# Kernel optimization log

Hardware: AMD Instinct MI355X
Metric: run time of the kernel (lower is better)

The kernel has to match this reference:

```python
import jax, jax.numpy as jnp
import numpy as np

N = 4096      # batch of RNA sequences
SEQ = 41      # hardcoded sequence length in the torch code
VEC = 15      # vector_length
T = 8         # target_length
EMB = 32      # embedding_dim of RNASequenceFilter.fc
LDIM = 256    # SequenceSplitter embedding_dim
RED = 64      # SequenceSplitter reduced_dim
BN_EPS = 1e-5


def setup_inputs() -> dict:
    key = jax.random.key(0)
    ks = jax.random.split(key, 20)
    A = jax.random.normal(ks[0], (N, SEQ, VEC), jnp.float32)
    start = jax.random.randint(ks[1], (N,), 0, 34)
    length = jax.random.randint(ks[2], (N,), 1, 9)  # region length in [1,8]
    C = jnp.stack([start, start + length - 1], axis=1).astype(jnp.int32)
    L = jax.random.normal(ks[3], (N, SEQ, LDIM), jnp.float32)
    s = 0.05
    return {
        "A": A, "C": C, "L": L,
        # RNASequenceFilter.fc : Linear(120,32) + Tanh + BatchNorm1d(32) (training mode)
        "W1": jax.random.normal(ks[4], (T * VEC, EMB), jnp.float32) * s,
        "b1": jnp.zeros((EMB,), jnp.float32),
        "bn_gamma": jnp.ones((EMB,), jnp.float32),
        "bn_beta": jnp.zeros((EMB,), jnp.float32),
        "sigma": jnp.float32(1.0),
        # SequenceSplitter lazy weights, initialized to ones
        "Pos_weights": jnp.ones((N, SEQ), jnp.float32),
        "Neg_weights": jnp.ones((N, SEQ), jnp.float32),
        # fc_pos
        "Wp1": jax.random.normal(ks[5], (LDIM, RED), jnp.float32) * s,
        "bp1": jnp.zeros((RED,), jnp.float32),
        "Wp2": jax.random.normal(ks[6], (RED, RED), jnp.float32) * s,
        "bp2": jnp.zeros((RED,), jnp.float32),
        # fc_neg
        "Wq1": jax.random.normal(ks[7], (LDIM, RED), jnp.float32) * s,
        "bq1": jnp.zeros((RED,), jnp.float32),
        "Wq2": jax.random.normal(ks[8], (RED, RED), jnp.float32) * s,
        "bq2": jnp.zeros((RED,), jnp.float32),
        # fc_all
        "Wa": jax.random.normal(ks[9], (LDIM, RED), jnp.float32) * s,
        "ba": jnp.zeros((RED,), jnp.float32),
    }


def _safe_cdist(x, y):
    # Euclidean cdist with zero (not NaN) gradient at zero distance.
    sq = (jnp.sum(x * x, -1)[:, None] + jnp.sum(y * y, -1)[None, :]
          - 2.0 * (x @ y.T))
    sq = jnp.maximum(sq, 0.0)
    safe = jnp.where(sq > 0.0, sq, 1.0)
    return jnp.where(sq > 0.0, jnp.sqrt(safe), 0.0)


def _forward(A, C, L, W1, b1, bn_gamma, bn_beta, sigma,
             Pos_weights, Neg_weights,
             Wp1, bp1, Wp2, bp2, Wq1, bq1, Wq2, bq2, Wa, ba):
    n = A.shape[0]
    start = C[:, 0].astype(jnp.int32)
    end = C[:, 1].astype(jnp.int32)
    length = end - start + 1  # [n], in [1, SEQ]

    # ---- build_graph: variable-length gather + linear interpolate (align_corners=False)
    j = jnp.arange(T, dtype=jnp.float32)
    scale = length.astype(jnp.float32)[:, None] / T          # [n,1]
    src = jnp.maximum(scale * (j + 0.5) - 0.5, 0.0)           # [n,T]
    i0 = jnp.minimum(jnp.floor(src).astype(jnp.int32), (length - 1)[:, None])
    i1 = jnp.minimum(i0 + 1, (length - 1)[:, None])
    w = src - i0.astype(jnp.float32)                          # lerp weight
    rows = jnp.arange(n)[:, None]
    g0 = A[rows, start[:, None] + i0]                         # [n,T,VEC]
    g1 = A[rows, start[:, None] + i1]
    key_regions = (1.0 - w)[..., None] * g0 + w[..., None] * g1
    flat = key_regions.reshape(n, T * VEC)

    h = jnp.tanh(flat @ W1 + b1)
    mu = h.mean(axis=0)
    var = ((h - mu) ** 2).mean(axis=0)                        # biased, training-mode BN
    emb = bn_gamma * (h - mu) * jax.lax.rsqrt(var + BN_EPS) + bn_beta

    D = jnp.exp(-_safe_cdist(emb, emb) / (2.0 * sigma ** 2))
    eye = jnp.eye(n, dtype=bool)
    off = ~eye
    avg = jnp.sum(jnp.where(off, D, 0.0)) / (n * (n - 1))
    D = jnp.where(D < avg, 0.0, D)
    mn = jnp.min(jnp.where(off, D, jnp.inf))
    mx = jnp.max(jnp.where(off, D, -jnp.inf))
    mx = jnp.where(mx == mn, mn + 1.0, mx)
    D = (D - mn) / (mx - mn)
    D = jnp.where(eye, 1.0, D)

    # ---- SequenceSplitter (only the paths feeding the outputs)
    idx = jnp.arange(SEQ)
    pmask = ((idx[None, :] >= start[:, None]) &
             (idx[None, :] <= end[:, None])).astype(L.dtype)  # [n,SEQ]
    pos_rep = (pmask * Pos_weights)[..., None] * L            # [n,SEQ,LDIM]
    neg_rep = ((1.0 - pmask) * Neg_weights)[..., None] * L

    key_t = jnp.tanh(jnp.tanh(pos_rep @ Wp1 + bp1) @ Wp2 + bp2)
    pos_vec = key_t.mean(axis=1)                              # [n,RED]
    nonkey_t = jnp.tanh(jnp.tanh(neg_rep @ Wq1 + bq1) @ Wq2 + bq2)
    neg_vec = nonkey_t.mean(axis=1)

    pos_sim = jnp.sum(jnp.exp(-_safe_cdist(pos_vec, pos_vec)))
    neg_sim = jnp.sum(jnp.exp(-_safe_cdist(pos_vec, neg_vec)))
    contrastive_loss = -jnp.log(pos_sim / neg_sim)

    final_feature = jnp.tanh((pos_rep + neg_rep) @ Wa + ba).mean(axis=1)  # [n,RED]
    return final_feature, contrastive_loss, D


def reference(A, C, L, W1, b1, bn_gamma, bn_beta, sigma,
              Pos_weights, Neg_weights,
              Wp1, bp1, Wp2, bp2, Wq1, bq1, Wq2, bq2, Wa, ba):
    return _forward(A, C, L, W1, b1, bn_gamma, bn_beta, sigma,
                    Pos_weights, Neg_weights,
                    Wp1, bp1, Wp2, bp2, Wq1, bq1, Wq2, bq2, Wa, ba)
```

## Files before the change

### kernel.cpp

```cpp
#include <hip/hip_runtime.h>
#include <cmath>

#define NN 4096
#define SEQ 41
#define VEC 15
#define TT 8
#define EMBD 32
#define LDIM 256
#define RED 64

#define WS_H       0
#define WS_CHUNKS  0
#define WS_EMB     524288
#define WS_SQN     1048576
#define WS_ROWSUM  1064960
#define WS_ROWMIN  1081344
#define WS_ROWMAX  1097728
#define WS_POSV    1114112
#define WS_NEGV    2162688
#define WS_STATS   3211264
#define WS_SIMS    3211520
#define WS_PAR     3211536

#define OUT_LOSS  (NN*RED)
#define OUT_D     (NN*RED + 1)

__global__ __launch_bounds__(64) void k_interp_h(
    const float* __restrict__ A, const int* __restrict__ C,
    const float* __restrict__ W1, const float* __restrict__ b1,
    float* __restrict__ h)
{
  __shared__ float flat[TT*VEC];
  const int n = blockIdx.x;
  const int t = threadIdx.x;
  const int st = C[2*n], en = C[2*n+1];
  const int len = en - st + 1;
  const float scale = __fdiv_rn((float)len, 8.0f);
  const float* Arow = A + ((size_t)n*SEQ + st) * VEC;
  for (int idx = t; idx < TT*VEC; idx += 64) {
    int j = idx / VEC, k = idx - j*VEC;
    float jf = (float)j + 0.5f;
    float src = fmaxf(__fsub_rn(__fmul_rn(scale, jf), 0.5f), 0.0f);
    int i0 = min((int)floorf(src), len-1);
    int i1 = min(i0+1, len-1);
    float w = __fsub_rn(src, (float)i0);
    float g0 = Arow[i0*VEC + k];
    float g1 = Arow[i1*VEC + k];
    flat[idx] = __fadd_rn(__fmul_rn(__fsub_rn(1.0f, w), g0), __fmul_rn(w, g1));
  }
  __syncthreads();
  if (t < EMBD) {
    float acc = 0.0f;
    #pragma unroll
    for (int i = 0; i < TT*VEC; i++) acc = __fmaf_rn(flat[i], W1[i*EMBD + t], acc);
    acc = __fadd_rn(acc, b1[t]);
    h[(size_t)n*EMBD + t] = (float)tanh((double)acc);
  }
}

#define BCH 128
__global__ __launch_bounds__(256) void k_bnstats(const float* __restrict__ h,
                                                 float* __restrict__ stats)
{
  __shared__ float tile[2][BCH*EMBD];
  __shared__ float smu[32];
  const int t = threadIdx.x;
  const int NCH = NN / BCH;

  {
    const float4* src = (const float4*)h;
    float4* dst = (float4*)tile[0];
    for (int v = t; v < BCH*8; v += 256) dst[v] = src[v];
  }
  __syncthreads();
  float acc = 0.0f;
  for (int c = 0; c < NCH; c++) {
    if (t >= 64 && c+1 < NCH) {
      const float4* src = (const float4*)(h + (size_t)(c+1)*BCH*EMBD);
      float4* dst = (float4*)tile[(c+1)&1];
      for (int v = t-64; v < BCH*8; v += 192) dst[v] = src[v];
    }
    if (t < 32) {
      const float* p = tile[c&1];
      #pragma unroll 8
      for (int r = 0; r < BCH; r++) acc = __fadd_rn(acc, p[r*EMBD + t]);
    }
    __syncthreads();
  }
  if (t < 32) smu[t] = __fdiv_rn(acc, 4096.0f);
  __syncthreads();

  {
    const float4* src = (const float4*)h;
    float4* dst = (float4*)tile[0];
    for (int v = t; v < BCH*8; v += 256) dst[v] = src[v];
  }
  __syncthreads();
  float q = 0.0f;
  for (int c = 0; c < NCH; c++) {
    if (t >= 64 && c+1 < NCH) {
      const float4* src = (const float4*)(h + (size_t)(c+1)*BCH*EMBD);
      float4* dst = (float4*)tile[(c+1)&1];
      for (int v = t-64; v < BCH*8; v += 192) dst[v] = src[v];
    }
    if (t < 32) {
      const float* p = tile[c&1];
      const float m = smu[t];
      #pragma unroll 8
      for (int r = 0; r < BCH; r++) {
        float d = __fsub_rn(p[r*EMBD + t], m);
        q = __fadd_rn(q, __fmul_rn(d, d));
      }
    }
    __syncthreads();
  }
  if (t < 32) {
    float var = __fdiv_rn(q, 4096.0f);
    stats[t] = smu[t];
    stats[32+t] = __fdiv_rn(1.0f, __fsqrt_rn(__fadd_rn(var, 1e-5f)));
  }
}

__global__ __launch_bounds__(256) void k_emb(
    const float* __restrict__ h, const float* __restrict__ stats,
    const float* __restrict__ gamma, const float* __restrict__ beta,
    float* __restrict__ emb, float* __restrict__ sqn,
    float* __restrict__ rowmin, float* __restrict__ rowmax)
{
  __shared__ float tile[8][32];
  const int t = threadIdx.x;
  const int r = t >> 5;
  const int e = t & 31;
  const int n = blockIdx.x*8 + r;
  float hv = h[(size_t)n*EMBD + e];
  float v = __fadd_rn(__fmul_rn(__fmul_rn(gamma[e], __fsub_rn(hv, stats[e])), stats[32+e]), beta[e]);
  emb[(size_t)n*EMBD + e] = v;
  tile[r][e] = v;
  __syncthreads();
  if (e == 0) {
    float sq[32];
    #pragma unroll
    for (int k = 0; k < 32; k++) { float x = tile[r][k]; sq[k] = __fmul_rn(x, x); }
    float rr[8];
    #pragma unroll
    for (int m = 0; m < 8; m++) rr[m] = sq[m];
    #pragma unroll
    for (int g = 1; g < 4; g++)
      #pragma unroll
      for (int m = 0; m < 8; m++) rr[m] = __fadd_rn(rr[m], sq[8*g + m]);
    float a = __fadd_rn(__fadd_rn(rr[0], rr[1]), __fadd_rn(rr[2], rr[3]));
    float b = __fadd_rn(__fadd_rn(rr[4], rr[5]), __fadd_rn(rr[6], rr[7]));
    sqn[n] = __fadd_rn(a, b);
    rowmin[n] = __int_as_float(0x7f800000);
    rowmax[n] = 0.0f;
  }
}

__device__ __forceinline__ float finishD(float dot, float ni, float nj, float denom)
{
  float t1 = __fadd_rn(ni, nj);
  float sq = __fsub_rn(t1, __fmul_rn(2.0f, dot));
  sq = fmaxf(sq, 0.0f);
  float dist = (sq > 0.0f) ? __fsqrt_rn(sq) : 0.0f;
  float q = __fdiv_rn(-dist, denom);
  return (float)exp((double)q);
}

#define TI 64
#define TJ 128
__global__ __launch_bounds__(256) void k_dtile(
    const float* __restrict__ emb, const float* __restrict__ sqn,
    const float* __restrict__ sigma, float* __restrict__ Dout,
    float* __restrict__ chunks, float* __restrict__ rowmin, float* __restrict__ rowmax)
{
  __shared__ __align__(16) float Ei[TI][36];
  __shared__ __align__(16) float Ej[TJ][36];
  const int t = threadIdx.x;
  const int bi = blockIdx.y;
  const int bj = blockIdx.x;
  const int jt = t & 15;
  const int it = t >> 4;

  {
    const float4* si = (const float4*)(emb + (size_t)bi*TI*EMBD);
    for (int v = t; v < TI*8; v += 256) {
      float4 x = si[v];
      *(float4*)&Ei[v >> 3][(v & 7) * 4] = x;
    }
    const float4* sj = (const float4*)(emb + (size_t)bj*TJ*EMBD);
    for (int v = t; v < TJ*8; v += 256) {
      float4 x = sj[v];
      *(float4*)&Ej[v >> 3][(v & 7) * 4] = x;
    }
  }

  const float s0 = sigma[0];
  const float denom = __fmul_rn(2.0f, __fmul_rn(s0, s0));

  float ni[4], nj[8];
  #pragma unroll
  for (int r = 0; r < 4; r++) ni[r] = sqn[bi*TI + it*4 + r];
  #pragma unroll
  for (int u = 0; u < 8; u++) nj[u] = sqn[bj*TJ + jt + 16*u];

  __syncthreads();

  float acc[4][8];
  #pragma unroll
  for (int r = 0; r < 4; r++)
    #pragma unroll
    for (int u = 0; u < 8; u++) acc[r][u] = 0.0f;

  #pragma unroll
  for (int kq = 0; kq < 8; kq++) {
    float4 a[4], b[8];
    #pragma unroll
    for (int r = 0; r < 4; r++) a[r] = *(const float4*)&Ei[it*4 + r][kq*4];
    #pragma unroll
    for (int u = 0; u < 8; u++) b[u] = *(const float4*)&Ej[jt + 16*u][kq*4];
    #pragma unroll
    for (int r = 0; r < 4; r++)
      #pragma unroll
      for (int u = 0; u < 8; u++) {
        float s = acc[r][u];
        s = __fmaf_rn(a[r].x, b[u].x, s);
        s = __fmaf_rn(a[r].y, b[u].y, s);
        s = __fmaf_rn(a[r].z, b[u].z, s);
        s = __fmaf_rn(a[r].w, b[u].w, s);
        acc[r][u] = s;
      }
  }

  const float PINF = __int_as_float(0x7f800000);
  const float NINF = __int_as_float(0xff800000);
  float wv[4][8];
  float thmn[4], thmx[4];
  #pragma unroll
  for (int r = 0; r < 4; r++) {
    const int ig = bi*TI + it*4 + r;
    float* Dr = Dout + (size_t)ig * NN + bj*TJ;
    float mn = PINF, mx = NINF;
    #pragma unroll
    for (int u = 0; u < 8; u++) {
      const int jg = bj*TJ + jt + 16*u;
      float Dv = finishD(acc[r][u], ni[r], nj[u], denom);
      const bool dg = (jg == ig);
      float wq = dg ? 0.0f : Dv;
      wv[r][u] = wq;
      Dr[jt + 16*u] = wq;
      mn = fminf(mn, dg ? PINF : Dv);
      mx = fmaxf(mx, dg ? NINF : Dv);
    }
    thmn[r] = mn; thmx[r] = mx;
  }

  #pragma unroll
  for (int r = 0; r < 4; r++) {
    float part[8];
    #pragma unroll
    for (int u = 0; u < 8; u++) part[u] = __shfl_xor(wv[r][u], 8, 16);
    float a = wv[r][0];
    a = __fadd_rn(a, part[0]);
    #pragma unroll
    for (int u = 1; u < 8; u++) {
      a = __fadd_rn(a, wv[r][u]);
      a = __fadd_rn(a, part[u]);
    }
    float s1 = __fadd_rn(a,  __shfl_xor(a, 1, 16));
    float s2 = __fadd_rn(s1, __shfl_xor(s1, 2, 16));
    float s3 = __fadd_rn(s2, __shfl_xor(s2, 4, 16));
    float mn = thmn[r], mx = thmx[r];
    #pragma unroll
    for (int m = 1; m < 16; m <<= 1) {
      mn = fminf(mn, __shfl_xor(mn, m, 16));
      mx = fmaxf(mx, __shfl_xor(mx, m, 16));
    }
    if (jt == 0) {
      const int ig = bi*TI + it*4 + r;
      chunks[(size_t)bj*NN + ig] = s3;
      atomicMin((int*)&rowmin[ig], __float_as_int(mn));
      atomicMax((int*)&rowmax[ig], __float_as_int(mx));
    }
  }
}

__global__ __launch_bounds__(256) void k_rowcombine(
    const float* __restrict__ chunks, float* __restrict__ rowsum,
    double* __restrict__ sims)
{
  const int i = blockIdx.x*256 + threadIdx.x;
  if (blockIdx.x == 0 && threadIdx.x == 0) { sims[0] = 0.0; sims[1] = 0.0; }
  float ch[32];
  #pragma unroll
  for (int c = 0; c < 32; c++) ch[c] = chunks[(size_t)c*NN + i];
  #pragma unroll
  for (int len = 32; len > 1; len >>= 1)
    #pragma unroll
    for (int k = 0; k < 16; k++)
      if (k < len/2) ch[k] = __fadd_rn(ch[2*k], ch[2*k+1]);
  rowsum[i] = ch[0];
}

__global__ __launch_bounds__(256) void k_dreduce(
    const float* __restrict__ rowsum, const float* __restrict__ rowmin,
    const float* __restrict__ rowmax, float* __restrict__ par)
{
  __shared__ float s[8192];
  __shared__ float rmn[256], rmx[256];
  const int t = threadIdx.x;
  for (int k = t; k < NN; k += 256) s[k] = rowsum[k];
  float mn = __int_as_float(0x7f800000), mx = __int_as_float(0xff800000);
  for (int k = t; k < NN; k += 256) {
    mn = fminf(mn, rowmin[k]);
    mx = fmaxf(mx, rowmax[k]);
  }
  rmn[t] = mn; rmx[t] = mx;
  __syncthreads();
  int src = 0, dst = 4096;
  for (int len = NN; len > 1; len >>= 1) {
    for (int k = t; k < len/2; k += 256)
      s[dst + k] = __fadd_rn(s[src + 2*k], s[src + 2*k+1]);
    __syncthreads();
    src = dst; dst = src + len/2;
  }
  for (int w = 128; w > 0; w >>= 1) {
    if (t < w) {
      rmn[t] = fminf(rmn[t], rmn[t+w]);
      rmx[t] = fmaxf(rmx[t], rmx[t+w]);
    }
    __syncthreads();
  }
  if (t == 0) {
    float S = s[src];
    float avg = __fdiv_rn(S, 16773120.0f);
    float mnr = rmn[0], mxr = rmx[0];
    float mnt = (mnr < avg) ? 0.0f : mnr;
    float mxt = (mxr < avg) ? 0.0f : mxr;
    if (mxt == mnt) mxt = __fadd_rn(mnt, 1.0f);
    par[0] = avg; par[1] = mnt; par[2] = __fsub_rn(mxt, mnt);
  }
}

__global__ __launch_bounds__(256) void k_dnorm(
    const float* __restrict__ par, float* __restrict__ D)
{
  const int i = blockIdx.x;
  const int t = threadIdx.x;
  const float avg = par[0], mnt = par[1], rng = par[2];
  float4* row = (float4*)(D + (size_t)i*NN);
  const int iv = i >> 2;
  for (int v = t; v < NN/4; v += 256) {
    float4 d = row[v];
    float o[4];
    float in[4] = {d.x, d.y, d.z, d.w};
    #pragma unroll
    for (int u = 0; u < 4; u++) {
      float val = (in[u] < avg) ? 0.0f : in[u];
      o[u] = __fdiv_rn(__fsub_rn(val, mnt), rng);
    }
    if (v == iv) o[i & 3] = 1.0f;
    row[v] = make_float4(o[0], o[1], o[2], o[3]);
  }
}

__global__ __launch_bounds__(256) void k_lpass(
    const float* __restrict__ L, const int* __restrict__ C,
    const float* __restrict__ PosW, const float* __restrict__ NegW,
    const float* __restrict__ Wp1, const float* __restrict__ bp1,
    const float* __restrict__ Wp2, const float* __restrict__ bp2,
    const float* __restrict__ Wq1, const float* __restrict__ bq1,
    const float* __restrict__ Wq2, const float* __restrict__ bq2,
    const float* __restrict__ Wa, const float* __restrict__ ba,
    float* __restrict__ out_ff, float* __restrict__ posv, float* __restrict__ negv)
{
  __shared__ __align__(16) float buf[SEQ*128];
  __shared__ float wps[SEQ], wns[SEQ];
  __shared__ float part[12*64];
  __shared__ __align__(16) float tb1[2*RED];

  float* apos = buf;
  float* aneg = buf + SEQ*RED;

  const int n = blockIdx.x;
  const int t = threadIdx.x;
  const int wu = __builtin_amdgcn_readfirstlane(t >> 6);
  const int lane = t & 63;

  const int st = C[2*n], en = C[2*n+1];

  if (t < SEQ) {
    bool pm = (t >= st && t <= en);
    wps[t] = pm ? PosW[(size_t)n*SEQ + t] : 0.0f;
    wns[t] = pm ? 0.0f : NegW[(size_t)n*SEQ + t];
  }
  if (t < RED) tb1[t] = tanhf(bp1[t]);
  else if (t < 2*RED) tb1[t] = tanhf(bq1[t - RED]);

  bool anyIn = false, anyOut = false;
  #pragma unroll
  for (int si = 0; si < 11; si++) {
    int s = wu + 4*si;
    if (s < SEQ) { bool r = (s >= st) && (s <= en); anyIn |= r; anyOut |= !r; }
  }

  float accs[11], acca[11];
  #pragma unroll
  for (int i = 0; i < 11; i++) { accs[i]=0.f; acca[i]=0.f; }

  const float4* Lg = (const float4*)(L + (size_t)n * (SEQ*LDIM));

  #pragma unroll
  for (int half = 0; half < 2; half++) {
    {
      float4* B4 = (float4*)buf;
      for (int v = t; v < SEQ*32; v += 256) {
        int s = v >> 5, c = v & 31;
        B4[v] = Lg[s*64 + half*32 + c];
      }
    }
    __syncthreads();
    const float* Wp1h = Wp1 + (size_t)half*128*RED + lane;
    const float* Wq1h = Wq1 + (size_t)half*128*RED + lane;
    const float* Wah  = Wa  + (size_t)half*128*RED + lane;
    for (int k0 = 0; k0 < 128; k0 += 4) {
      float wpr[4], wqr[4], war[4];
      if (anyIn) {
        #pragma unroll
        for (int kk = 0; kk < 4; kk++) wpr[kk] = Wp1h[(k0+kk)*RED];
      }
      if (anyOut) {
        #pragma unroll
        for (int kk = 0; kk < 4; kk++) wqr[kk] = Wq1h[(k0+kk)*RED];
      }
      #pragma unroll
      for (int kk = 0; kk < 4; kk++) war[kk] = Wah[(k0+kk)*RED];
      #pragma unroll
      for (int si = 0; si < 11; si++) {
        const int s = wu + 4*si;
        if (s < SEQ) {
          const bool inr = (s >= st) && (s <= en);
          float4 l4 = *(const float4*)&buf[s*128 + k0];
          if (inr) {
            accs[si] = __fmaf_rn(l4.x, wpr[0], accs[si]);
            accs[si] = __fmaf_rn(l4.y, wpr[1], accs[si]);
            accs[si] = __fmaf_rn(l4.z, wpr[2], accs[si]);
            accs[si] = __fmaf_rn(l4.w, wpr[3], accs[si]);
          } else {
            accs[si] = __fmaf_rn(l4.x, wqr[0], accs[si]);
            accs[si] = __fmaf_rn(l4.y, wqr[1], accs[si]);
            accs[si] = __fmaf_rn(l4.z, wqr[2], accs[si]);
            accs[si] = __fmaf_rn(l4.w, wqr[3], accs[si]);
          }
          acca[si] = __fmaf_rn(l4.x, war[0], acca[si]);
          acca[si] = __fmaf_rn(l4.y, war[1], acca[si]);
          acca[si] = __fmaf_rn(l4.z, war[2], acca[si]);
          acca[si] = __fmaf_rn(l4.w, war[3], acca[si]);
        }
      }
    }
    __syncthreads();
  }

  const float bpl = bp1[lane], bql = bq1[lane], bal = ba[lane];
  float ffl = 0.f;
  #pragma unroll
  for (int si = 0; si < 11; si++) {
    const int s = wu + 4*si;
    if (s < SEQ) {
      const bool inr = (s >= st) && (s <= en);
      if (inr) {
        float wp = wps[s];
        apos[s*RED + lane] = tanhf(__fmaf_rn(wp, accs[si], bpl));
        ffl += tanhf(__fmaf_rn(wp, acca[si], bal));
      } else {
        float wn = wns[s];
        aneg[s*RED + lane] = tanhf(__fmaf_rn(wn, accs[si], bql));
        ffl += tanhf(__fmaf_rn(wn, acca[si], bal));
      }
    }
  }
  part[(0*4 + wu)*64 + lane] = ffl;
  __syncthreads();

  float acc2[11];
  float c2p = 0.f, c2q = 0.f;
  #pragma unroll
  for (int i = 0; i < 11; i++) acc2[i] = 0.f;
  const float* Wp2l = Wp2 + lane;
  const float* Wq2l = Wq2 + lane;
  for (int k0 = 0; k0 < RED; k0 += 4) {
    float p2[4], q2[4];
    #pragma unroll
    for (int kk = 0; kk < 4; kk++) {
      p2[kk] = Wp2l[(k0+kk)*RED];
      q2[kk] = Wq2l[(k0+kk)*RED];
    }
    float4 tp = *(const float4*)&tb1[k0];
    float4 tq = *(const float4*)&tb1[RED + k0];
    c2p = __fmaf_rn(tp.x, p2[0], c2p);
    c2p = __fmaf_rn(tp.y, p2[1], c2p);
    c2p = __fmaf_rn(tp.z, p2[2], c2p);
    c2p = __fmaf_rn(tp.w, p2[3], c2p);
    c2q = __fmaf_rn(tq.x, q2[0], c2q);
    c2q = __fmaf_rn(tq.y, q2[1], c2q);
    c2q = __fmaf_rn(tq.z, q2[2], c2q);
    c2q = __fmaf_rn(tq.w, q2[3], c2q);
    #pragma unroll
    for (int si = 0; si < 11; si++) {
      const int s = wu + 4*si;
      if (s < SEQ) {
        const bool inr = (s >= st) && (s <= en);
        if (inr) {
          float4 a4 = *(const float4*)&apos[s*RED + k0];
          acc2[si] = __fmaf_rn(a4.x, p2[0], acc2[si]);
          acc2[si] = __fmaf_rn(a4.y, p2[1], acc2[si]);
          acc2[si] = __fmaf_rn(a4.z, p2[2], acc2[si]);
          acc2[si] = __fmaf_rn(a4.w, p2[3], acc2[si]);
        } else {
          float4 b4 = *(const float4*)&aneg[s*RED + k0];
          acc2[si] = __fmaf_rn(b4.x, q2[0], acc2[si]);
          acc2[si] = __fmaf_rn(b4.y, q2[1], acc2[si]);
          acc2[si] = __fmaf_rn(b4.z, q2[2], acc2[si]);
          acc2[si] = __fmaf_rn(b4.w, q2[3], acc2[si]);
        }
      }
    }
  }
  const float bp2l = bp2[lane], bq2l = bq2[lane];
  const float tcp = tanhf(__fadd_rn(c2p, bp2l));
  const float tcq = tanhf(__fadd_rn(c2q, bq2l));
  float pl = 0.f, nl = 0.f;
  int nin = 0, nval = 0;
  #pragma unroll
  for (int si = 0; si < 11; si++) {
    const int s = wu + 4*si;
    if (s < SEQ) {
      nval++;
      const bool inr = (s >= st) && (s <= en);
      if (inr) {
        nin++;
        pl += tanhf(__fadd_rn(acc2[si], bp2l));
      } else {
        nl += tanhf(__fadd_rn(acc2[si], bq2l));
      }
    }
  }
  pl += (float)(nval - nin) * tcp;
  nl += (float)nin * tcq;
  part[(1*4 + wu)*64 + lane] = pl;
  part[(2*4 + wu)*64 + lane] = nl;
  __syncthreads();

  if (wu == 0) {
    float s = part[0*256 + 0*64 + lane] + part[0*256 + 1*64 + lane]
            + part[0*256 + 2*64 + lane] + part[0*256 + 3*64 + lane];
    out_ff[(size_t)n*RED + lane] = s * (1.0f/41.0f);
  } else if (wu == 1) {
    float s = part[1*256 + 0*64 + lane] + part[1*256 + 1*64 + lane]
            + part[1*256 + 2*64 + lane] + part[1*256 + 3*64 + lane];
    posv[(size_t)n*RED + lane] = s * (1.0f/41.0f);
  } else if (wu == 2) {
    float s = part[2*256 + 0*64 + lane] + part[2*256 + 1*64 + lane]
            + part[2*256 + 2*64 + lane] + part[2*256 + 3*64 + lane];
    negv[(size_t)n*RED + lane] = s * (1.0f/41.0f);
  }
}

__global__ __launch_bounds__(256) void k_sim(
    const float* __restrict__ posv, const float* __restrict__ negv,
    double* __restrict__ sims)
{
  __shared__ float xI[64*64];
  __shared__ float yJ[64*65];
  __shared__ float nxs[64];
  __shared__ double wsum[4];
  const int which = blockIdx.z;
  const int bi = blockIdx.x, bj = blockIdx.y, t = threadIdx.x;
  if (which == 0 && bi > bj) return;
  const float* X = posv;
  const float* Y = which ? negv : posv;
  {
    const float4* X4 = (const float4*)(X + (size_t)(bi*64)*RED);
    float4* xI4 = (float4*)xI;
    for (int v = t; v < 1024; v += 256) xI4[v] = X4[v];
  }
  for (int v = t; v < 4096; v += 256) {
    int r = v >> 6, c = v & 63;
    yJ[r*65+c] = Y[(size_t)(bj*64+r)*RED + c];
  }
  __syncthreads();
  if (t < 64) {
    float s = 0.f;
    #pragma unroll
    for (int k = 0; k < 64; k++) { float v = xI[t*64+k]; s += v*v; }
    nxs[t] = s;
  }
  const int jl = t & 63, iq = t >> 6;
  float yv[64];
  #pragma unroll
  for (int k = 0; k < 64; k++) yv[k] = yJ[jl*65+k];
  float ny = 0.f;
  #pragma unroll
  for (int k = 0; k < 64; k++) ny += yv[k]*yv[k];
  __syncthreads();
  double lsum = 0.0;
  for (int ii = 0; ii < 16; ii++) {
    int il = iq*16 + ii;
    float dot = 0.f;
    #pragma unroll
    for (int k = 0; k < 64; k += 4) {
      float4 x = *(const float4*)&xI[il*64+k];
      dot += x.x*yv[k] + x.y*yv[k+1] + x.z*yv[k+2] + x.w*yv[k+3];
    }
    float sq = fmaxf(nxs[il] + ny - 2.0f*dot, 0.0f);
    float dist = (sq > 0.f) ? sqrtf(sq) : 0.f;
    lsum += (double)expf(-dist);
  }
  #pragma unroll
  for (int m = 32; m >= 1; m >>= 1) lsum += __shfl_down(lsum, m);
  if ((t & 63) == 0) wsum[t>>6] = lsum;
  __syncthreads();
  if (t == 0) {
    double mult = (which == 0 && bi < bj) ? 2.0 : 1.0;
    atomicAdd(&sims[which], mult*(wsum[0]+wsum[1]+wsum[2]+wsum[3]));
  }
}

__global__ void k_loss(const double* __restrict__ sims, float* __restrict__ out_loss) {
  out_loss[0] = (float)(-log(sims[0]/sims[1]));
}

extern "C" void kernel_launch(void* const* d_in, const int* in_sizes, int n_in,
                              void* d_out, int out_size, void* d_ws, size_t ws_size,
                              hipStream_t stream) {
  const float* A     = (const float*)d_in[0];
  const int*   C     = (const int*)  d_in[1];
  const float* L     = (const float*)d_in[2];
  const float* W1    = (const float*)d_in[3];
  const float* b1    = (const float*)d_in[4];
  const float* gamma = (const float*)d_in[5];
  const float* beta  = (const float*)d_in[6];
  const float* sigma = (const float*)d_in[7];
  const float* PosW  = (const float*)d_in[8];
  const float* NegW  = (const float*)d_in[9];
  const float* Wp1   = (const float*)d_in[10];
  const float* bp1   = (const float*)d_in[11];
  const float* Wp2   = (const float*)d_in[12];
  const float* bp2   = (const float*)d_in[13];
  const float* Wq1   = (const float*)d_in[14];
  const float* bq1   = (const float*)d_in[15];
  const float* Wq2   = (const float*)d_in[16];
  const float* bq2   = (const float*)d_in[17];
  const float* Wa    = (const float*)d_in[18];
  const float* ba    = (const float*)d_in[19];

  float* out = (float*)d_out;
  char* ws = (char*)d_ws;
  float* h      = (float*)(ws + WS_H);
  float* chunks = (float*)(ws + WS_CHUNKS);
  float* emb    = (float*)(ws + WS_EMB);
  float* sqn    = (float*)(ws + WS_SQN);
  float* rowsum = (float*)(ws + WS_ROWSUM);
  float* rowmin = (float*)(ws + WS_ROWMIN);
  float* rowmax = (float*)(ws + WS_ROWMAX);
  float* posv   = (float*)(ws + WS_POSV);
  float* negv   = (float*)(ws + WS_NEGV);
  float* stats  = (float*)(ws + WS_STATS);
  double* sims  = (double*)(ws + WS_SIMS);
  float* par    = (float*)(ws + WS_PAR);

  hipLaunchKernelGGL(k_interp_h, dim3(NN), dim3(64), 0, stream, A, C, W1, b1, h);
  hipLaunchKernelGGL(k_bnstats, dim3(1), dim3(256), 0, stream, h, stats);
  hipLaunchKernelGGL(k_emb, dim3(NN/8), dim3(256), 0, stream, h, stats, gamma, beta, emb, sqn, rowmin, rowmax);
  hipLaunchKernelGGL(k_dtile, dim3(NN/TJ, NN/TI), dim3(256), 0, stream, emb, sqn, sigma, out + OUT_D, chunks, rowmin, rowmax);
  hipLaunchKernelGGL(k_rowcombine, dim3(16), dim3(256), 0, stream, chunks, rowsum, sims);
  hipLaunchKernelGGL(k_dreduce, dim3(1), dim3(256), 0, stream, rowsum, rowmin, rowmax, par);
  hipLaunchKernelGGL(k_dnorm, dim3(NN), dim3(256), 0, stream, par, out + OUT_D);
  hipLaunchKernelGGL(k_lpass, dim3(NN), dim3(256), 0, stream,
                     L, C, PosW, NegW, Wp1, bp1, Wp2, bp2, Wq1, bq1, Wq2, bq2, Wa, ba,
                     out, posv, negv);
  hipLaunchKernelGGL(k_sim, dim3(64,64,2), dim3(256), 0, stream, posv, negv, sims);
  hipLaunchKernelGGL(k_loss, dim3(1), dim3(1), 0, stream, sims, out + OUT_LOSS);
}
```

Measured before the change: 942.3 us.

## Compact in-region and out-region rows into index lists in k_lpass

k_lpass now builds per-block index lists of in-region and out-of-region sequence positions, padded with a zero dummy row. Each wave processes fixed-size lists: 2 positive rows and 10 negative rows. This removes the per-row branch that chose between the Wp and Wq paths in both layers. The padded slots contribute known tanh-of-bias terms, and the final reductions correct for them with constant offsets (33*tcp for the positive side, tcq for the negative side). In exchange, the code always loads both Wp1 and Wq1, does slightly more redundant FMA work on the padded rows, uses more registers, and does a serial list build on one thread.

After: 885.9 us. 6.0% less time.

```diff
diff --git a/kernel.cpp b/kernel.cpp
--- a/kernel.cpp
+++ b/kernel.cpp
@@ -373,17 +373,18 @@
     const float* __restrict__ Wa, const float* __restrict__ ba,
     float* __restrict__ out_ff, float* __restrict__ posv, float* __restrict__ negv)
 {
-  __shared__ __align__(16) float buf[SEQ*128];
-  __shared__ float wps[SEQ], wns[SEQ];
+  __shared__ __align__(16) float buf[42*128];
+  __shared__ float wps[SEQ+1], wns[SEQ+1];
   __shared__ float part[12*64];
   __shared__ __align__(16) float tb1[2*RED];
+  __shared__ int inIdx[8], outIdx[40];
 
   float* apos = buf;
-  float* aneg = buf + SEQ*RED;
+  float* aneg = buf + 42*RED;
 
   const int n = blockIdx.x;
   const int t = threadIdx.x;
-  const int wu = __builtin_amdgcn_readfirstlane(t >> 6);
+  const int w = t >> 6;
   const int lane = t & 63;
 
   const int st = C[2*n], en = C[2*n+1];
@@ -392,22 +393,32 @@
     bool pm = (t >= st && t <= en);
     wps[t] = pm ? PosW[(size_t)n*SEQ + t] : 0.0f;
     wns[t] = pm ? 0.0f : NegW[(size_t)n*SEQ + t];
+  } else if (t == SEQ) {
+    wps[SEQ] = 0.0f; wns[SEQ] = 0.0f;
   }
   if (t < RED) tb1[t] = tanhf(bp1[t]);
   else if (t < 2*RED) tb1[t] = tanhf(bq1[t - RED]);
-
-  bool anyIn = false, anyOut = false;
-  #pragma unroll
-  for (int si = 0; si < 11; si++) {
-    int s = wu + 4*si;
-    if (s < SEQ) { bool r = (s >= st) && (s <= en); anyIn |= r; anyOut |= !r; }
-  }
-
-  float accs[11], acca[11];
-  #pragma unroll
-  for (int i = 0; i < 11; i++) { accs[i]=0.f; acca[i]=0.f; }
+  if (t == 255) {
+    int ci = 0;
+    for (int s = st; s <= en; s++) inIdx[ci++] = s;
+    while (ci < 8) inIdx[ci++] = SEQ;
+    int co = 0;
+    for (int s = 0; s < st; s++) outIdx[co++] = s;
+    for (int s = en+1; s < SEQ; s++) outIdx[co++] = s;
+    while (co < 40) outIdx[co++] = SEQ;
+  }
+
+  float accp[2], accq[10], acca[11];
+  #pragma unroll
+  for (int i = 0; i < 2; i++) accp[i] = 0.f;
+  #pragma unroll
+  for (int i = 0; i < 10; i++) accq[i] = 0.f;
+  #pragma unroll
+  for (int i = 0; i < 11; i++) acca[i] = 0.f;
 
   const float4* Lg = (const float4*)(L + (size_t)n * (SEQ*LDIM));
+
+  int sIn[2], sOut[10];
 
   #pragma unroll
   for (int half = 0; half < 2; half++) {
@@ -417,40 +428,46 @@
         int s = v >> 5, c = v & 31;
         B4[v] = Lg[s*64 + half*32 + c];
       }
+      if (t < 32) B4[SEQ*32 + t] = make_float4(0.f, 0.f, 0.f, 0.f);
     }
     __syncthreads();
+    if (half == 0) {
+      sIn[0] = inIdx[w]; sIn[1] = inIdx[w + 4];
+      #pragma unroll
+      for (int i = 0; i < 10; i++) sOut[i] = outIdx[w + 4*i];
+    }
     const float* Wp1h = Wp1 + (size_t)half*128*RED + lane;
     const float* Wq1h = Wq1 + (size_t)half*128*RED + lane;
     const float* Wah  = Wa  + (size_t)half*128*RED + lane;
     for (int k0 = 0; k0 < 128; k0 += 4) {
       float wpr[4], wqr[4], war[4];
-      if (anyIn) {
-        #pragma unroll
-        for (int kk = 0; kk < 4; kk++) wpr[kk] = Wp1h[(k0+kk)*RED];
-      }
-      if (anyOut) {
-        #pragma unroll
-        for (int kk = 0; kk < 4; kk++) wqr[kk] = Wq1h[(k0+kk)*RED];
+      #pragma unroll
+      for (int kk = 0; kk < 4; kk++) {
+        wpr[kk] = Wp1h[(k0+kk)*RED];
+        wqr[kk] = Wq1h[(k0+kk)*RED];
+        war[kk] = Wah [(k0+kk)*RED];
       }
       #pragma unroll
-      for (int kk = 0; kk < 4; kk++) war[kk] = Wah[(k0+kk)*RED];
+      for (int io = 0; io < 2; io++) {
+        float4 l4 = *(const float4*)&buf[sIn[io]*128 + k0];
+        accp[io] = __fmaf_rn(l4.x, wpr[0], accp[io]);
+        accp[io] = __fmaf_rn(l4.y, wpr[1], accp[io]);
+        accp[io] = __fmaf_rn(l4.z, wpr[2], accp[io]);
+        accp[io] = __fmaf_rn(l4.w, wpr[3], accp[io]);
+      }
+      #pragma unroll
+      for (int oo = 0; oo < 10; oo++) {
+        float4 l4 = *(const float4*)&buf[sOut[oo]*128 + k0];
+        accq[oo] = __fmaf_rn(l4.x, wqr[0], accq[oo]);
+        accq[oo] = __fmaf_rn(l4.y, wqr[1], accq[oo]);
+        accq[oo] = __fmaf_rn(l4.z, wqr[2], accq[oo]);
+        accq[oo] = __fmaf_rn(l4.w, wqr[3], accq[oo]);
+      }
       #pragma unroll
       for (int si = 0; si < 11; si++) {
-        const int s = wu + 4*si;
+        int s = w + 4*si;
         if (s < SEQ) {
-          const bool inr = (s >= st) && (s <= en);
           float4 l4 = *(const float4*)&buf[s*128 + k0];
-          if (inr) {
-            accs[si] = __fmaf_rn(l4.x, wpr[0], accs[si]);
-            accs[si] = __fmaf_rn(l4.y, wpr[1], accs[si]);
-            accs[si] = __fmaf_rn(l4.z, wpr[2], accs[si]);
-            accs[si] = __fmaf_rn(l4.w, wpr[3], accs[si]);
-          } else {
-            accs[si] = __fmaf_rn(l4.x, wqr[0], accs[si]);
-            accs[si] = __fmaf_rn(l4.y, wqr[1], accs[si]);
-            accs[si] = __fmaf_rn(l4.z, wqr[2], accs[si]);
-            accs[si] = __fmaf_rn(l4.w, wqr[3], accs[si]);
-          }
           acca[si] = __fmaf_rn(l4.x, war[0], acca[si]);
           acca[si] = __fmaf_rn(l4.y, war[1], acca[si]);
           acca[si] = __fmaf_rn(l4.z, war[2], acca[si]);
@@ -464,28 +481,29 @@
   const float bpl = bp1[lane], bql = bq1[lane], bal = ba[lane];
   float ffl = 0.f;
   #pragma unroll
+  for (int io = 0; io < 2; io++) {
+    int s = sIn[io];
+    apos[s*RED + lane] = tanhf(__fmaf_rn(wps[s], accp[io], bpl));
+  }
+  #pragma unroll
+  for (int oo = 0; oo < 10; oo++) {
+    int s = sOut[oo];
+    aneg[s*RED + lane] = tanhf(__fmaf_rn(wns[s], accq[oo], bql));
+  }
+  #pragma unroll
   for (int si = 0; si < 11; si++) {
-    const int s = wu + 4*si;
-    if (s < SEQ) {
-      const bool inr = (s >= st) && (s <= en);
-      if (inr) {
-        float wp = wps[s];
-        apos[s*RED + lane] = tanhf(__fmaf_rn(wp, accs[si], bpl));
-        ffl += tanhf(__fmaf_rn(wp, acca[si], bal));
-      } else {
-        float wn = wns[s];
-        aneg[s*RED + lane] = tanhf(__fmaf_rn(wn, accs[si], bql));
-        ffl += tanhf(__fmaf_rn(wn, acca[si], bal));
-      }
-    }
-  }
-  part[(0*4 + wu)*64 + lane] = ffl;
-  __syncthreads();
-
-  float acc2[11];
+    int s = w + 4*si;
+    if (s < SEQ) ffl += tanhf(__fmaf_rn(wps[s] + wns[s], acca[si], bal));
+  }
+  part[(0*4 + w)*64 + lane] = ffl;
+  __syncthreads();
+
+  float accP[2], accQ[10];
   float c2p = 0.f, c2q = 0.f;
   #pragma unroll
-  for (int i = 0; i < 11; i++) acc2[i] = 0.f;
+  for (int i = 0; i < 2; i++) accP[i] = 0.f;
+  #pragma unroll
+  for (int i = 0; i < 10; i++) accQ[i] = 0.f;
   const float* Wp2l = Wp2 + lane;
   const float* Wq2l = Wq2 + lane;
   for (int k0 = 0; k0 < RED; k0 += 4) {
@@ -506,62 +524,47 @@
     c2q = __fmaf_rn(tq.z, q2[2], c2q);
     c2q = __fmaf_rn(tq.w, q2[3], c2q);
     #pragma unroll
-    for (int si = 0; si < 11; si++) {
-      const int s = wu + 4*si;
-      if (s < SEQ) {
-        const bool inr = (s >= st) && (s <= en);
-        if (inr) {
-          float4 a4 = *(const float4*)&apos[s*RED + k0];
-          acc2[si] = __fmaf_rn(a4.x, p2[0], acc2[si]);
-          acc2[si] = __fmaf_rn(a4.y, p2[1], acc2[si]);
-          acc2[si] = __fmaf_rn(a4.z, p2[2], acc2[si]);
-          acc2[si] = __fmaf_rn(a4.w, p2[3], acc2[si]);
-        } else {
-          float4 b4 = *(const float4*)&aneg[s*RED + k0];
-          acc2[si] = __fmaf_rn(b4.x, q2[0], acc2[si]);
-          acc2[si] = __fmaf_rn(b4.y, q2[1], acc2[si]);
-          acc2[si] = __fmaf_rn(b4.z, q2[2], acc2[si]);
-          acc2[si] = __fmaf_rn(b4.w, q2[3], acc2[si]);
-        }
-      }
+    for (int io = 0; io < 2; io++) {
+      float4 a4 = *(const float4*)&apos[sIn[io]*RED + k0];
+      accP[io] = __fmaf_rn(a4.x, p2[0], accP[io]);
+      accP[io] = __fmaf_rn(a4.y, p2[1], accP[io]);
+      accP[io] = __fmaf_rn(a4.z, p2[2], accP[io]);
+      accP[io] = __fmaf_rn(a4.w, p2[3], accP[io]);
+    }
+    #pragma unroll
+    for (int oo = 0; oo < 10; oo++) {
+      float4 b4 = *(const float4*)&aneg[sOut[oo]*RED + k0];
+      accQ[oo] = __fmaf_rn(b4.x, q2[0], accQ[oo]);
+      accQ[oo] = __fmaf_rn(b4.y, q2[1], accQ[oo]);
+      accQ[oo] = __fmaf_rn(b4.z, q2[2], accQ[oo]);
+      accQ[oo] = __fmaf_rn(b4.w, q2[3], accQ[oo]);
     }
   }
   const float bp2l = bp2[lane], bq2l = bq2[lane];
   const float tcp = tanhf(__fadd_rn(c2p, bp2l));
   const float tcq = tanhf(__fadd_rn(c2q, bq2l));
   float pl = 0.f, nl = 0.f;
-  int nin = 0, nval = 0;
-  #pragma unroll
-  for (int si = 0; si < 11; si++) {
-    const int s = wu + 4*si;
-    if (s < SEQ) {
-      nval++;
-      const bool inr = (s >= st) && (s <= en);
-      if (inr) {
-        nin++;
-        pl += tanhf(__fadd_rn(acc2[si], bp2l));
-      } else {
-        nl += tanhf(__fadd_rn(acc2[si], bq2l));
-      }
-    }
-  }
-  pl += (float)(nval - nin) * tcp;
-  nl += (float)nin * tcq;
-  part[(1*4 + wu)*64 + lane] = pl;
-  part[(2*4 + wu)*64 + lane] = nl;
-  __syncthreads();
-
-  if (wu == 0) {
+  #pragma unroll
+  for (int io = 0; io < 2; io++) pl += tanhf(__fadd_rn(accP[io], bp2l));
+  #pragma unroll
+  for (int oo = 0; oo < 10; oo++) nl += tanhf(__fadd_rn(accQ[oo], bq2l));
+  part[(1*4 + w)*64 + lane] = pl;
+  part[(2*4 + w)*64 + lane] = nl;
+  __syncthreads();
+
+  if (w == 0) {
     float s = part[0*256 + 0*64 + lane] + part[0*256 + 1*64 + lane]
             + part[0*256 + 2*64 + lane] + part[0*256 + 3*64 + lane];
     out_ff[(size_t)n*RED + lane] = s * (1.0f/41.0f);
-  } else if (wu == 1) {
+  } else if (w == 1) {
     float s = part[1*256 + 0*64 + lane] + part[1*256 + 1*64 + lane]
             + part[1*256 + 2*64 + lane] + part[1*256 + 3*64 + lane];
+    s += 33.0f * tcp;
     posv[(size_t)n*RED + lane] = s * (1.0f/41.0f);
-  } else if (wu == 2) {
+  } else if (w == 2) {
     float s = part[2*256 + 0*64 + lane] + part[2*256 + 1*64 + lane]
             + part[2*256 + 2*64 + lane] + part[2*256 + 3*64 + lane];
+    s += tcq;
     negv[(size_t)n*RED + lane] = s * (1.0f/41.0f);
   }
 }
```
